# Performance work log

Hardware: AMD Instinct MI355X
Metric: run time of the kernel (lower is better)

The kernel has to match this reference:

```python
import math
import jax, jax.numpy as jnp
import numpy as np

G = 128        # graphs per batch
N0 = 512       # nodes per graph
H = 256        # hidden size
E = 524288     # edges (avg degree 8), intra-graph
RATIO = 0.8


def setup_inputs() -> dict:
    key = jax.random.key(0)
    ks = jax.random.split(key, 16)
    # intra-graph edges: E//G edges per graph
    eg = jnp.arange(E, dtype=jnp.int32) // (E // G)
    src = eg * N0 + jax.random.randint(ks[0], (E,), 0, N0, dtype=jnp.int32)
    dst = eg * N0 + jax.random.randint(ks[1], (E,), 0, N0, dtype=jnp.int32)
    s = 1.0 / math.sqrt(H)
    return {
        "x": jax.random.normal(ks[2], (G * N0, H), jnp.float32),
        "edge_src": src,
        "edge_dst": dst,
        "W_in": jax.random.normal(ks[3], (H, H), jnp.float32) * s,
        "b_in": jnp.zeros((H,), jnp.float32),
        "W_h0": jax.random.normal(ks[4], (H, H), jnp.float32) * s,
        "b_h0": jnp.zeros((H,), jnp.float32),
        "W_h1": jax.random.normal(ks[5], (H, H), jnp.float32) * s,
        "b_h1": jnp.zeros((H,), jnp.float32),
        "p_in": jax.random.normal(ks[6], (H,), jnp.float32),
        "p_h0": jax.random.normal(ks[7], (H,), jnp.float32),
        "p_h1": jax.random.normal(ks[8], (H,), jnp.float32),
        "att_w": jax.random.normal(ks[9], (H,), jnp.float32) * s,
        "att_b": jnp.zeros((1,), jnp.float32),
    }


def gcn_conv(x, W, b, src, dst, emask, num_nodes):
    # PyG GCNConv: lin -> sym-normalized propagate (with self loops, weight 1) -> bias
    h = x @ W
    deg = jax.ops.segment_sum(emask, dst, num_segments=num_nodes) + 1.0  # +1 self loop
    dis = jax.lax.rsqrt(deg)
    coef = dis[src] * dis[dst] * emask                    # [E]
    agg = jax.ops.segment_sum(h[src] * coef[:, None], dst, num_segments=num_nodes)
    agg = agg + h * (dis * dis)[:, None]                  # self-loop message
    return agg + b


def topk_pool(x, p, src, dst, emask, n_cur):
    # PyG TopKPooling: score = tanh(x.p/|p|), keep top ceil(ratio*n) per graph,
    # x' = x[perm]*score[perm], edges filtered to kept nodes and remapped.
    k = int(math.ceil(RATIO * n_cur))
    score = jnp.tanh((x @ p) / jnp.linalg.norm(p))        # [G*n_cur]
    _, idx = jax.lax.top_k(score.reshape(G, n_cur), k)    # [G,k]
    perm = (idx + (jnp.arange(G, dtype=idx.dtype) * n_cur)[:, None]).reshape(-1)
    x_new = x[perm] * score[perm][:, None]                # [G*k,H]
    mapping = jnp.full((G * n_cur,), -1, jnp.int32).at[perm].set(
        jnp.arange(G * k, dtype=jnp.int32))
    ns, nd = mapping[src], mapping[dst]
    valid = (ns >= 0) & (nd >= 0) & (emask > 0)
    return (x_new, jnp.where(valid, ns, 0), jnp.where(valid, nd, 0),
            valid.astype(x.dtype), k)


def att_pool(x, att_w, att_b, k):
    # GlobalAttention: per-graph softmax gate, weighted sum
    gate = (x @ att_w + att_b[0]).reshape(G, k)
    att = jax.nn.softmax(gate, axis=1)
    return jnp.einsum('gk,gkh->gh', att, x.reshape(G, k, H))


def reference(x, edge_src, edge_dst, W_in, b_in, W_h0, b_h0, W_h1, b_h1,
              p_in, p_h0, p_h1, att_w, att_b):
    src, dst = edge_src, edge_dst
    emask = jnp.ones((E,), x.dtype)
    n_cur = N0
    h = jax.nn.relu(gcn_conv(x, W_in, b_in, src, dst, emask, G * n_cur))
    h, src, dst, emask, n_cur = topk_pool(h, p_in, src, dst, emask, n_cur)
    out = att_pool(h, att_w, att_b, n_cur)
    for (W, b, p) in ((W_h0, b_h0, p_h0), (W_h1, b_h1, p_h1)):
        h = jax.nn.relu(gcn_conv(h, W, b, src, dst, emask, G * n_cur))
        h, src, dst, emask, n_cur = topk_pool(h, p, src, dst, emask, n_cur)
        out = out + att_pool(h, att_w, att_b, n_cur)
    return out  # [G, H]
```

## Files before the change

### kernel.cpp

```cpp
#include <hip/hip_runtime.h>
#include <cmath>

#define G_ 128
#define N0_ 512
#define H_ 256
#define E_ 524288
#define NODES0 (G_*N0_)

typedef _Float16 v8h __attribute__((ext_vector_type(8)));
typedef _Float16 v4h __attribute__((ext_vector_type(4)));
typedef float v4f __attribute__((ext_vector_type(4)));

#define TSTRIDE 72
#define TILEHW (128*TSTRIDE)

__device__ __forceinline__ void async_copy16(void* lds, const void* g) {
  __builtin_amdgcn_global_load_lds(
      (const __attribute__((address_space(1))) void*)g,
      (__attribute__((address_space(3))) void*)lds, 16, 0, 0);
}

__device__ __forceinline__ float4 f4fma(float4 a, float s, float4 acc) {
  acc.x = fmaf(a.x, s, acc.x); acc.y = fmaf(a.y, s, acc.y);
  acc.z = fmaf(a.z, s, acc.z); acc.w = fmaf(a.w, s, acc.w);
  return acc;
}

__device__ __forceinline__ float block_reduce_sum(float v, volatile float* red) {
  #pragma unroll
  for (int off = 32; off > 0; off >>= 1) v += __shfl_down(v, off);
  int lane = threadIdx.x & 63, wid = threadIdx.x >> 6;
  __syncthreads();
  if (lane == 0) red[wid] = v;
  __syncthreads();
  return red[0] + red[1] + red[2] + red[3];
}

__global__ __launch_bounds__(256) void pnorm_kernel(const float* __restrict__ p0,
                                                    const float* __restrict__ p1,
                                                    const float* __restrict__ p2,
                                                    float* __restrict__ pinv) {
  __shared__ float red[4];
  const float* p = (blockIdx.x == 0) ? p0 : (blockIdx.x == 1 ? p1 : p2);
  float v = p[threadIdx.x];
  float s = block_reduce_sum(v * v, red);
  if (threadIdx.x == 0) pinv[blockIdx.x] = 1.0f / sqrtf(s);
}

__global__ void init_kernel(int* __restrict__ cum, int* __restrict__ orig_of,
                            int* __restrict__ cnt, int n) {
  int v = blockIdx.x * 256 + threadIdx.x;
  if (v < n) { cum[v] = v; orig_of[v] = v; cnt[v] = 0; }
}

__global__ __launch_bounds__(256) void wconv_kernel(const float* __restrict__ W0,
                                                    const float* __restrict__ W1,
                                                    const float* __restrict__ W2,
                                                    _Float16* __restrict__ img) {
  int l = blockIdx.x >> 4;
  const float* W = (l == 0) ? W0 : (l == 1 ? W1 : W2);
  int bn = (blockIdx.x >> 3) & 1, kt = blockIdx.x & 7;
  int t = threadIdx.x;
  int n = t & 127, kh = t >> 7;
  int k0 = kt * 32 + kh * 16;
  _Float16* row = img + (size_t)l * 16 * TILEHW + ((size_t)(bn * 8 + kt) * 128 + n) * TSTRIDE;
  #pragma unroll
  for (int s = 0; s < 2; ++s) {
    v8h hv, lv;
    #pragma unroll
    for (int j = 0; j < 8; ++j) {
      float a = W[(size_t)(k0 + s * 8 + j) * 256 + bn * 128 + n];
      _Float16 h = (_Float16)a;
      hv[j] = h;
      lv[j] = (_Float16)(a - (float)h);
    }
    *(v8h*)&row[kh * 16 + s * 8] = hv;
    *(v8h*)&row[32 + kh * 16 + s * 8] = lv;
  }
}

__global__ void count0_kernel(const int* __restrict__ edst, int* __restrict__ cnt) {
  int e = blockIdx.x * 256 + threadIdx.x;
  if (e < E_) atomicAdd(&cnt[edst[e]], 1);
}

__global__ __launch_bounds__(256) void scan1_kernel(const int* __restrict__ cnt,
                                                    int* __restrict__ row0,
                                                    int* __restrict__ bsum,
                                                    float* __restrict__ dis,
                                                    int* __restrict__ cursor, int n) {
  __shared__ int sdata[256];
  int base = blockIdx.x * 1024;
  int t = threadIdx.x;
  int v[4]; int s = 0;
  #pragma unroll
  for (int i = 0; i < 4; ++i) {
    int idx = base + t * 4 + i;
    v[i] = (idx < n) ? cnt[idx] : 0;
    s += v[i];
    if (idx < n) {
      dis[idx] = 1.0f / sqrtf((float)v[i] + 1.0f);
      cursor[idx] = 0;
    }
  }
  sdata[t] = s;
  __syncthreads();
  for (int off = 1; off < 256; off <<= 1) {
    int x = (t >= off) ? sdata[t - off] : 0;
    __syncthreads();
    sdata[t] += x;
    __syncthreads();
  }
  int excl = sdata[t] - s;
  if (t == 255) bsum[blockIdx.x] = sdata[255];
  #pragma unroll
  for (int i = 0; i < 4; ++i) {
    int idx = base + t * 4 + i;
    if (idx < n) { row0[idx] = excl; excl += v[i]; }
  }
}

__global__ __launch_bounds__(256) void scan2_kernel(int* __restrict__ bsum,
                                                    int* __restrict__ row0, int nb, int n) {
  __shared__ int sdata[256];
  int t = threadIdx.x;
  int v = (t < nb) ? bsum[t] : 0;
  sdata[t] = v;
  __syncthreads();
  for (int off = 1; off < 256; off <<= 1) {
    int x = (t >= off) ? sdata[t - off] : 0;
    __syncthreads();
    sdata[t] += x;
    __syncthreads();
  }
  if (t < nb) bsum[t] = sdata[t] - v;
  if (t == 255) row0[n] = sdata[255];
}

__global__ void fill0_kernel(const int* __restrict__ esrc, const int* __restrict__ edst,
                             const int* __restrict__ row0, const int* __restrict__ bsum,
                             int* __restrict__ cursor, int* __restrict__ csr0) {
  int e = blockIdx.x * 256 + threadIdx.x;
  if (e >= E_) return;
  int d = edst[e];
  int pos = atomicAdd(&cursor[d], 1);
  csr0[row0[d] + bsum[d >> 10] + pos] = esrc[e];
}

__global__ void deg_kernel(const int* __restrict__ orig_of, const int* __restrict__ row0,
                           const int* __restrict__ bsum, const int* __restrict__ csr0,
                           const int* __restrict__ cum, float* __restrict__ dis, int nodes) {
  int v = blockIdx.x * 256 + threadIdx.x;
  if (v >= nodes) return;
  int o = orig_of[v];
  int rs = row0[o] + bsum[o >> 10];
  int o1 = o + 1;
  int re = row0[o1] + ((o1 < NODES0) ? bsum[o1 >> 10] : 0);
  int c = 0;
  for (int j = rs; j < re; ++j) c += (cum[csr0[j]] >= 0) ? 1 : 0;
  dis[v] = rsqrtf((float)c + 1.0f);
}

__global__ __launch_bounds__(256) void gemm_f16x3_kernel(const float* __restrict__ A,
                                                         const int* __restrict__ perm,
                                                         const float* __restrict__ score,
                                                         const _Float16* __restrict__ Wimg,
                                                         float* __restrict__ C) {
  __shared__ _Float16 As[TILEHW];
  __shared__ _Float16 Ws[TILEHW];
  const int tid = threadIdx.x;
  const int bm = blockIdx.x >> 1;
  const int bn = blockIdx.x & 1;
  const int lane = tid & 63, wid = tid >> 6;
  const int wm = wid >> 1, wn = wid & 1;
  const int l15 = lane & 15, kg = lane >> 4;

  v4f acc[4][4];
  #pragma unroll
  for (int i = 0; i < 4; ++i)
    #pragma unroll
    for (int j = 0; j < 4; ++j) acc[i][j] = (v4f){0.f, 0.f, 0.f, 0.f};

  int arow[4], acc4[4];
  const float* aptr[4];
  float ascale[4];
  #pragma unroll
  for (int i = 0; i < 4; ++i) {
    int c = tid + 256 * i;
    arow[i] = c >> 3;
    acc4[i] = c & 7;
    int R = bm * 128 + arow[i];
    int pr = perm ? perm[R] : R;
    ascale[i] = perm ? score[pr] : 1.0f;
    aptr[i] = A + (size_t)pr * 256 + acc4[i] * 4;
  }
  const _Float16* wtile0 = Wimg + (size_t)bn * 8 * TILEHW;

  float4 pa[4];
  #pragma unroll
  for (int i = 0; i < 4; ++i) pa[i] = *(const float4*)(aptr[i] + 0);

  for (int kt = 0; kt < 8; ++kt) {
    {
      const _Float16* wt = wtile0 + (size_t)kt * TILEHW;
      for (int cb = wid; cb < 18; cb += 4)
        async_copy16(&Ws[cb * 512], wt + (size_t)cb * 512 + lane * 8);
    }
    #pragma unroll
    for (int i = 0; i < 4; ++i) {
      float av[4] = {pa[i].x * ascale[i], pa[i].y * ascale[i],
                     pa[i].z * ascale[i], pa[i].w * ascale[i]};
      v4h hv, lv;
      #pragma unroll
      for (int j = 0; j < 4; ++j) {
        _Float16 h = (_Float16)av[j];
        hv[j] = h;
        lv[j] = (_Float16)(av[j] - (float)h);
      }
      _Float16* dst = &As[arow[i] * TSTRIDE + acc4[i] * 4];
      *(v4h*)(dst) = hv;
      *(v4h*)(dst + 32) = lv;
    }
    __syncthreads();

    if (kt < 7) {
      #pragma unroll
      for (int i = 0; i < 4; ++i)
        pa[i] = *(const float4*)(aptr[i] + (kt + 1) * 32);
    }

    v8h ah[4], bh[4], al[4], bl[4];
    #pragma unroll
    for (int i = 0; i < 4; ++i)
      ah[i] = *(const v8h*)&As[(wm * 64 + i * 16 + l15) * TSTRIDE + kg * 8];
    #pragma unroll
    for (int j = 0; j < 4; ++j)
      bh[j] = *(const v8h*)&Ws[(wn * 64 + j * 16 + l15) * TSTRIDE + kg * 8];
    #pragma unroll
    for (int i = 0; i < 4; ++i)
      #pragma unroll
      for (int j = 0; j < 4; ++j)
        acc[i][j] = __builtin_amdgcn_mfma_f32_16x16x32_f16(ah[i], bh[j], acc[i][j], 0, 0, 0);
    #pragma unroll
    for (int i = 0; i < 4; ++i)
      al[i] = *(const v8h*)&As[(wm * 64 + i * 16 + l15) * TSTRIDE + 32 + kg * 8];
    #pragma unroll
    for (int i = 0; i < 4; ++i)
      #pragma unroll
      for (int j = 0; j < 4; ++j)
        acc[i][j] = __builtin_amdgcn_mfma_f32_16x16x32_f16(al[i], bh[j], acc[i][j], 0, 0, 0);
    #pragma unroll
    for (int j = 0; j < 4; ++j)
      bl[j] = *(const v8h*)&Ws[(wn * 64 + j * 16 + l15) * TSTRIDE + 32 + kg * 8];
    #pragma unroll
    for (int i = 0; i < 4; ++i)
      #pragma unroll
      for (int j = 0; j < 4; ++j)
        acc[i][j] = __builtin_amdgcn_mfma_f32_16x16x32_f16(ah[i], bl[j], acc[i][j], 0, 0, 0);
    __syncthreads();
  }

  #pragma unroll
  for (int i = 0; i < 4; ++i) {
    #pragma unroll
    for (int j = 0; j < 4; ++j) {
      #pragma unroll
      for (int r = 0; r < 4; ++r) {
        int row = bm * 128 + wm * 64 + i * 16 + kg * 4 + r;
        int col = bn * 128 + wn * 64 + j * 16 + l15;
        C[(size_t)row * 256 + col] = acc[i][j][r];
      }
    }
  }
}

__global__ __launch_bounds__(256) void agg_score_kernel(
    const float4* __restrict__ hlin4, const float* __restrict__ dis,
    const float4* __restrict__ bias4,
    const int* __restrict__ orig_of, const int* __restrict__ row0,
    const int* __restrict__ bsum, const int* __restrict__ csr0,
    const int* __restrict__ cum,
    const float4* __restrict__ p4, const float* __restrict__ pinvp,
    float4* __restrict__ hout4, float* __restrict__ score, int q) {
  int blk = (blockIdx.x & 7) * q + (blockIdx.x >> 3);
  int wave = threadIdx.x >> 6, lane = threadIdx.x & 63;
  int v = blk * 4 + wave;
  float dv = dis[v];
  float self = dv * dv;
  float4 h = hlin4[(size_t)v * 64 + lane];
  float4 acc = make_float4(h.x * self, h.y * self, h.z * self, h.w * self);
  int o = orig_of[v];
  int rs = row0[o] + bsum[o >> 10];
  int o1 = o + 1;
  int re = row0[o1] + ((o1 < NODES0) ? bsum[o1 >> 10] : 0);
  int j = rs;
  while (j < re) {
    int mrem = re - j;
    int c[8]; float cf[8];
    #pragma unroll
    for (int u = 0; u < 8; ++u) {
      if (u < mrem) {
        int cc = cum[csr0[j + u]];
        c[u] = cc;
        cf[u] = (cc >= 0) ? dis[cc] * dv : 0.0f;
      } else c[u] = -1;
    }
    float4 hh[8];
    #pragma unroll
    for (int u = 0; u < 8; ++u)
      if (c[u] >= 0) hh[u] = hlin4[(size_t)c[u] * 64 + lane];
    #pragma unroll
    for (int u = 0; u < 8; ++u)
      if (c[u] >= 0) acc = f4fma(hh[u], cf[u], acc);
    j += (mrem < 8) ? mrem : 8;
  }
  float4 b = bias4[lane];
  acc.x = fmaxf(acc.x + b.x, 0.0f); acc.y = fmaxf(acc.y + b.y, 0.0f);
  acc.z = fmaxf(acc.z + b.z, 0.0f); acc.w = fmaxf(acc.w + b.w, 0.0f);
  hout4[(size_t)v * 64 + lane] = acc;
  float4 pv = p4[lane];
  float s = acc.x * pv.x + acc.y * pv.y + acc.z * pv.z + acc.w * pv.w;
  #pragma unroll
  for (int off = 32; off > 0; off >>= 1) s += __shfl_down(s, off);
  if (lane == 0) score[v] = tanhf(s * pinvp[0]);
}

__global__ __launch_bounds__(256) void topk_kernel(const float* __restrict__ score, int n, int k,
                                                   int* __restrict__ cum,
                                                   const int* __restrict__ orig_prev,
                                                   int* __restrict__ orig_new,
                                                   int* __restrict__ perm) {
  __shared__ float key[512];
  __shared__ int kid[512];
  __shared__ int newmap[512];
  int g = blockIdx.x, t = threadIdx.x;
  for (int i = t; i < 512; i += 256) {
    key[i] = (i < n) ? score[(size_t)g * n + i] : -INFINITY;
    kid[i] = i;
    if (i < n) newmap[i] = -1;
  }
  __syncthreads();
  for (int kk = 2; kk <= 512; kk <<= 1) {
    for (int j = kk >> 1; j > 0; j >>= 1) {
      #pragma unroll
      for (int half = 0; half < 2; ++half) {
        int i = t + half * 256;
        int ixj = i ^ j;
        if (ixj > i) {
          float ka = key[i]; int ia = kid[i];
          float kb = key[ixj]; int ib = kid[ixj];
          bool b_first = (kb > ka) || (kb == ka && ib < ia);
          bool sw = ((i & kk) == 0) ? b_first : !b_first;
          if (sw) { key[i] = kb; kid[i] = ib; key[ixj] = ka; kid[ixj] = ia; }
        }
      }
      __syncthreads();
    }
  }
  for (int i = t; i < k; i += 256) {
    int local = kid[i];
    perm[g * k + i] = g * n + local;
    newmap[local] = g * k + i;
    orig_new[g * k + i] = orig_prev[g * n + local];
  }
  __syncthreads();
  #pragma unroll
  for (int u = 0; u < N0_ / 256; ++u) {
    int v = g * N0_ + u * 256 + t;
    int c = cum[v];
    if (c >= 0) cum[v] = newmap[c - g * n];
  }
}

__global__ __launch_bounds__(512) void pool_kernel(
    const float4* __restrict__ h4, const float* __restrict__ score,
    const int* __restrict__ perm,
    const float4* __restrict__ attw4, const float* __restrict__ attb,
    float* __restrict__ out, int k, int add) {
  __shared__ float wmax[8], wsum[8];
  __shared__ float4 waccs[8][64];
  int g = blockIdx.x, t = threadIdx.x;
  int wave = t >> 6, lane = t & 63;
  float4 aw = attw4[lane];
  float ab = attb[0];

  float m = -INFINITY, ssum = 0.0f;
  float4 acc = make_float4(0.f, 0.f, 0.f, 0.f);
  for (int i = wave; i < k; i += 8) {
    int s = perm[g * k + i];
    float sc = score[s];
    float4 hv = h4[(size_t)s * 64 + lane];
    float4 val = make_float4(hv.x * sc, hv.y * sc, hv.z * sc, hv.w * sc);
    float gd = val.x * aw.x + val.y * aw.y + val.z * aw.z + val.w * aw.w;
    #pragma unroll
    for (int off = 32; off > 0; off >>= 1) gd += __shfl_xor(gd, off);
    float gi = gd + ab;
    float mnew = fmaxf(m, gi);
    float f = __expf(m - mnew);
    float e = __expf(gi - mnew);
    acc.x = acc.x * f + val.x * e; acc.y = acc.y * f + val.y * e;
    acc.z = acc.z * f + val.z * e; acc.w = acc.w * f + val.w * e;
    ssum = ssum * f + e;
    m = mnew;
  }
  if (lane == 0) { wmax[wave] = m; wsum[wave] = ssum; }
  waccs[wave][lane] = acc;
  __syncthreads();
  if (wave == 0) {
    float mstar = wmax[0];
    #pragma unroll
    for (int w = 1; w < 8; ++w) mstar = fmaxf(mstar, wmax[w]);
    float stot = 0.0f;
    float4 a = make_float4(0.f, 0.f, 0.f, 0.f);
    #pragma unroll
    for (int w = 0; w < 8; ++w) {
      float sc = __expf(wmax[w] - mstar);
      stot += wsum[w] * sc;
      float4 wa = waccs[w][lane];
      a.x += wa.x * sc; a.y += wa.y * sc; a.z += wa.z * sc; a.w += wa.w * sc;
    }
    float inv = 1.0f / stot;
    a.x *= inv; a.y *= inv; a.z *= inv; a.w *= inv;
    float4* o4 = (float4*)out + (size_t)g * 64 + lane;
    if (add) {
      float4 prev = *o4;
      a.x += prev.x; a.y += prev.y; a.z += prev.z; a.w += prev.w;
    }
    *o4 = a;
  }
}

extern "C" void kernel_launch(void* const* d_in, const int* in_sizes, int n_in,
                              void* d_out, int out_size, void* d_ws, size_t ws_size,
                              hipStream_t stream) {
  const float* x    = (const float*)d_in[0];
  const int*   esrc = (const int*)d_in[1];
  const int*   edst = (const int*)d_in[2];
  const float* Wl[3] = {(const float*)d_in[3], (const float*)d_in[5], (const float*)d_in[7]};
  const float* bl[3] = {(const float*)d_in[4], (const float*)d_in[6], (const float*)d_in[8]};
  const float* pl[3] = {(const float*)d_in[9], (const float*)d_in[10], (const float*)d_in[11]};
  const float* attw = (const float*)d_in[12];
  const float* attb = (const float*)d_in[13];
  float* out = (float*)d_out;

  char* w = (char*)d_ws;
  auto carve = [&](size_t bytes) { char* p = w; w += (bytes + 255) & ~(size_t)255; return p; };
  float* bufA    = (float*)carve((size_t)NODES0 * H_ * 4);
  float* bufB    = (float*)carve((size_t)NODES0 * H_ * 4);
  int*   csr0    = (int*)  carve((size_t)E_ * 4);
  int*   cnt     = (int*)  carve((size_t)NODES0 * 4);
  int*   row0    = (int*)  carve((size_t)(NODES0 + 1) * 4);
  int*   cursor  = (int*)  carve((size_t)NODES0 * 4);
  float* dis     = (float*)carve((size_t)NODES0 * 4);
  float* score   = (float*)carve((size_t)NODES0 * 4);
  int*   cum_map = (int*)  carve((size_t)NODES0 * 4);
  int*   origA   = (int*)  carve((size_t)NODES0 * 4);
  int*   origB   = (int*)  carve((size_t)NODES0 * 4);
  int*   perm    = (int*)  carve((size_t)NODES0 * 4);
  int*   bsum    = (int*)  carve(256 * 4);
  float* pinv    = (float*)carve(16);
  _Float16* Wimg = (_Float16*)carve((size_t)3 * 16 * TILEHW * 2);
  (void)ws_size; (void)in_sizes; (void)n_in; (void)out_size;

  pnorm_kernel<<<3, 256, 0, stream>>>(pl[0], pl[1], pl[2], pinv);
  init_kernel<<<NODES0 / 256, 256, 0, stream>>>(cum_map, origA, cnt, NODES0);
  wconv_kernel<<<48, 256, 0, stream>>>(Wl[0], Wl[1], Wl[2], Wimg);

  count0_kernel<<<E_ / 256, 256, 0, stream>>>(edst, cnt);
  int nb0 = (NODES0 + 1023) / 1024;
  scan1_kernel<<<nb0, 256, 0, stream>>>(cnt, row0, bsum, dis, cursor, NODES0);
  scan2_kernel<<<1, 256, 0, stream>>>(bsum, row0, nb0, NODES0);
  fill0_kernel<<<E_ / 256, 256, 0, stream>>>(esrc, edst, row0, bsum, cursor, csr0);

  int n_cur = N0_;
  int* origs[2] = {origA, origB};
  for (int l = 0; l < 3; ++l) {
    int nodes = G_ * n_cur;
    int* orig_cur = origs[l & 1];
    int* orig_nxt = origs[(l & 1) ^ 1];

    if (l > 0) {
      deg_kernel<<<(nodes + 255) / 256, 256, 0, stream>>>(orig_cur, row0, bsum, csr0,
                                                          cum_map, dis, nodes);
    }

    gemm_f16x3_kernel<<<(nodes / 128) * 2, 256, 0, stream>>>(
        (l == 0) ? x : bufB, (l == 0) ? nullptr : perm, score,
        Wimg + (size_t)l * 16 * TILEHW, bufA);

    int agg_blocks = nodes / 4;
    agg_score_kernel<<<agg_blocks, 256, 0, stream>>>(
        (const float4*)bufA, dis, (const float4*)bl[l], orig_cur, row0, bsum, csr0,
        cum_map, (const float4*)pl[l], pinv + l, (float4*)bufB, score, agg_blocks / 8);

    int kk = (int)std::ceil(0.8 * (double)n_cur);
    topk_kernel<<<G_, 256, 0, stream>>>(score, n_cur, kk, cum_map, orig_cur, orig_nxt, perm);

    pool_kernel<<<G_, 512, 0, stream>>>(
        (const float4*)bufB, score, perm, (const float4*)attw, attb, out, kk, l > 0 ? 1 : 0);

    n_cur = kk;
  }
}
```

Baseline: 466.1 us.

## Precompute per-edge remapped sources and normalization coefficients for aggregation

```diff
diff --git a/kernel.cpp b/kernel.cpp
--- a/kernel.cpp
+++ b/kernel.cpp
@@ -139,12 +139,17 @@
 
 __global__ void fill0_kernel(const int* __restrict__ esrc, const int* __restrict__ edst,
                              const int* __restrict__ row0, const int* __restrict__ bsum,
-                             int* __restrict__ cursor, int* __restrict__ csr0) {
+                             int* __restrict__ cursor, const float* __restrict__ dis,
+                             int* __restrict__ csr0, int* __restrict__ csr_dst,
+                             float* __restrict__ cf0) {
   int e = blockIdx.x * 256 + threadIdx.x;
   if (e >= E_) return;
-  int d = edst[e];
+  int d = edst[e], s = esrc[e];
   int pos = atomicAdd(&cursor[d], 1);
-  csr0[row0[d] + bsum[d >> 10] + pos] = esrc[e];
+  int idx = row0[d] + bsum[d >> 10] + pos;
+  csr0[idx] = s;
+  csr_dst[idx] = d;
+  cf0[idx] = dis[s] * dis[d];
 }
 
 __global__ void deg_kernel(const int* __restrict__ orig_of, const int* __restrict__ row0,
@@ -159,6 +164,18 @@
   int c = 0;
   for (int j = rs; j < re; ++j) c += (cum[csr0[j]] >= 0) ? 1 : 0;
   dis[v] = rsqrtf((float)c + 1.0f);
+}
+
+__global__ void remap_kernel(const int* __restrict__ csr0, const int* __restrict__ csr_dst,
+                             const int* __restrict__ cum, const float* __restrict__ dis,
+                             int* __restrict__ src_l, float* __restrict__ cf_l) {
+  int j = blockIdx.x * 256 + threadIdx.x;
+  if (j >= E_) return;
+  int md = cum[csr_dst[j]];
+  if (md < 0) return;
+  int ms = cum[csr0[j]];
+  src_l[j] = (ms >= 0) ? ms : 0;
+  cf_l[j] = (ms >= 0) ? dis[ms] * dis[md] : 0.0f;
 }
 
 __global__ __launch_bounds__(256) void gemm_f16x3_kernel(const float* __restrict__ A,
@@ -278,8 +295,8 @@
     const float4* __restrict__ hlin4, const float* __restrict__ dis,
     const float4* __restrict__ bias4,
     const int* __restrict__ orig_of, const int* __restrict__ row0,
-    const int* __restrict__ bsum, const int* __restrict__ csr0,
-    const int* __restrict__ cum,
+    const int* __restrict__ bsum,
+    const int* __restrict__ src_arr, const float* __restrict__ cf_arr,
     const float4* __restrict__ p4, const float* __restrict__ pinvp,
     float4* __restrict__ hout4, float* __restrict__ score, int q) {
   int blk = (blockIdx.x & 7) * q + (blockIdx.x >> 3);
@@ -294,25 +311,27 @@
   int o1 = o + 1;
   int re = row0[o1] + ((o1 < NODES0) ? bsum[o1 >> 10] : 0);
   int j = rs;
-  while (j < re) {
-    int mrem = re - j;
-    int c[8]; float cf[8];
-    #pragma unroll
-    for (int u = 0; u < 8; ++u) {
-      if (u < mrem) {
-        int cc = cum[csr0[j + u]];
-        c[u] = cc;
-        cf[u] = (cc >= 0) ? dis[cc] * dv : 0.0f;
-      } else c[u] = -1;
-    }
-    float4 hh[8];
-    #pragma unroll
-    for (int u = 0; u < 8; ++u)
-      if (c[u] >= 0) hh[u] = hlin4[(size_t)c[u] * 64 + lane];
-    #pragma unroll
-    for (int u = 0; u < 8; ++u)
-      if (c[u] >= 0) acc = f4fma(hh[u], cf[u], acc);
-    j += (mrem < 8) ? mrem : 8;
+  for (; j + 8 <= re; j += 8) {
+    int s[8]; float c[8]; float4 hh[8];
+    #pragma unroll
+    for (int u = 0; u < 8; ++u) { s[u] = src_arr[j + u]; c[u] = cf_arr[j + u]; }
+    #pragma unroll
+    for (int u = 0; u < 8; ++u) hh[u] = hlin4[(size_t)s[u] * 64 + lane];
+    #pragma unroll
+    for (int u = 0; u < 8; ++u) acc = f4fma(hh[u], c[u], acc);
+  }
+  if (j + 4 <= re) {
+    int s[4]; float c[4]; float4 hh[4];
+    #pragma unroll
+    for (int u = 0; u < 4; ++u) { s[u] = src_arr[j + u]; c[u] = cf_arr[j + u]; }
+    #pragma unroll
+    for (int u = 0; u < 4; ++u) hh[u] = hlin4[(size_t)s[u] * 64 + lane];
+    #pragma unroll
+    for (int u = 0; u < 4; ++u) acc = f4fma(hh[u], c[u], acc);
+    j += 4;
+  }
+  for (; j < re; ++j) {
+    acc = f4fma(hlin4[(size_t)src_arr[j] * 64 + lane], cf_arr[j], acc);
   }
   float4 b = bias4[lane];
   acc.x = fmaxf(acc.x + b.x, 0.0f); acc.y = fmaxf(acc.y + b.y, 0.0f);
@@ -448,6 +467,10 @@
   float* bufA    = (float*)carve((size_t)NODES0 * H_ * 4);
   float* bufB    = (float*)carve((size_t)NODES0 * H_ * 4);
   int*   csr0    = (int*)  carve((size_t)E_ * 4);
+  int*   csr_dst = (int*)  carve((size_t)E_ * 4);
+  float* cf0     = (float*)carve((size_t)E_ * 4);
+  int*   src_l   = (int*)  carve((size_t)E_ * 4);
+  float* cf_l    = (float*)carve((size_t)E_ * 4);
   int*   cnt     = (int*)  carve((size_t)NODES0 * 4);
   int*   row0    = (int*)  carve((size_t)(NODES0 + 1) * 4);
   int*   cursor  = (int*)  carve((size_t)NODES0 * 4);
@@ -470,7 +493,8 @@
   int nb0 = (NODES0 + 1023) / 1024;
   scan1_kernel<<<nb0, 256, 0, stream>>>(cnt, row0, bsum, dis, cursor, NODES0);
   scan2_kernel<<<1, 256, 0, stream>>>(bsum, row0, nb0, NODES0);
-  fill0_kernel<<<E_ / 256, 256, 0, stream>>>(esrc, edst, row0, bsum, cursor, csr0);
+  fill0_kernel<<<E_ / 256, 256, 0, stream>>>(esrc, edst, row0, bsum, cursor, dis,
+                                             csr0, csr_dst, cf0);
 
   int n_cur = N0_;
   int* origs[2] = {origA, origB};
@@ -482,6 +506,7 @@
     if (l > 0) {
       deg_kernel<<<(nodes + 255) / 256, 256, 0, stream>>>(orig_cur, row0, bsum, csr0,
                                                           cum_map, dis, nodes);
+      remap_kernel<<<E_ / 256, 256, 0, stream>>>(csr0, csr_dst, cum_map, dis, src_l, cf_l);
     }
 
     gemm_f16x3_kernel<<<(nodes / 128) * 2, 256, 0, stream>>>(
@@ -490,8 +515,9 @@
 
     int agg_blocks = nodes / 4;
     agg_score_kernel<<<agg_blocks, 256, 0, stream>>>(
-        (const float4*)bufA, dis, (const float4*)bl[l], orig_cur, row0, bsum, csr0,
-        cum_map, (const float4*)pl[l], pinv + l, (float4*)bufB, score, agg_blocks / 8);
+        (const float4*)bufA, dis, (const float4*)bl[l], orig_cur, row0, bsum,
+        (l == 0) ? csr0 : src_l, (l == 0) ? cf0 : cf_l,
+        (const float4*)pl[l], pinv + l, (float4*)bufB, score, agg_blocks / 8);
 
     int kk = (int)std::ceil(0.8 * (double)n_cur);
     topk_kernel<<<G_, 256, 0, stream>>>(score, n_cur, kk, cum_map, orig_cur, orig_nxt, perm);
```

Measured after the change: 411.2 us. 1.13x faster.
